# Optimization experiments

Hardware: AMD Instinct MI355X
Metric: run time of the kernel (lower is better)

## Reference

```python
import jax, jax.numpy as jnp
import numpy as np

HIDDEN = 1024
HEADS = 16
HEAD_DIM = HIDDEN // HEADS
ROPE_THETA = 10000.0
WINDOW = 128
NEG_INF = -1e9


def _rope_cos_sin(seq_len, head_dim, theta, dtype):
    # inv_freq: [dh/2]; emb = concat([freqs, freqs]) to match rotate-half convention
    inv_freq = 1.0 / (theta ** (jnp.arange(0, head_dim, 2, dtype=jnp.float32) / head_dim))
    pos = jnp.arange(seq_len, dtype=jnp.float32)
    freqs = jnp.einsum('s,d->sd', pos, inv_freq)          # [S, dh/2]
    emb = jnp.concatenate([freqs, freqs], axis=-1)        # [S, dh]
    return jnp.cos(emb).astype(dtype), jnp.sin(emb).astype(dtype)


def _apply_rope(x, cos, sin):
    # x: [B, S, H, dh]; cos/sin: [S, dh] broadcast over batch and heads
    x1, x2 = jnp.split(x, 2, axis=-1)
    half_rot = jnp.concatenate([-x2, x1], axis=-1)
    c = cos[None, :, None, :]
    s = sin[None, :, None, :]
    return x * c + half_rot * s


def setup_inputs() -> dict:
    key = jax.random.key(0)
    k1, k2, k3, k4, k5 = jax.random.split(key, 5)
    std = 0.02
    return {
        'hidden_states': jax.random.normal(k1, (2, 2048, HIDDEN), dtype=jnp.float32),
        'Wq': jax.random.normal(k2, (HIDDEN, HEADS, HEAD_DIM), dtype=jnp.float32) * std,
        'Wk': jax.random.normal(k3, (HIDDEN, HEADS, HEAD_DIM), dtype=jnp.float32) * std,
        'Wv': jax.random.normal(k4, (HIDDEN, HEADS, HEAD_DIM), dtype=jnp.float32) * std,
        'Wo': jax.random.normal(k5, (HEADS, HEAD_DIM, HIDDEN), dtype=jnp.float32) * std,
    }


def reference(hidden_states, Wq, Wk, Wv, Wo):
    B, S, D = hidden_states.shape
    x4 = hidden_states.reshape(B, S, HEADS, HEAD_DIM)
    cos, sin = _rope_cos_sin(S, HEAD_DIM, ROPE_THETA, hidden_states.dtype)
    # RoPE applied to raw hidden states (pre-projection), per original module
    q_in = _apply_rope(x4, cos, sin).reshape(B, S, D)
    k_in = q_in  # query and key get identical RoPE of the same tensor
    v_in = hidden_states

    q = jnp.einsum('bsd,dhk->bshk', q_in, Wq)  # [B,S,H,dh]
    k = jnp.einsum('bsd,dhk->bshk', k_in, Wk)
    v = jnp.einsum('bsd,dhk->bshk', v_in, Wv)

    scale = 1.0 / jnp.sqrt(jnp.asarray(HEAD_DIM, dtype=q.dtype))
    scores = jnp.einsum('bqhd,bkhd->bhqk', q, k) * scale  # [B,H,S,S]

    # sliding-window mask: |i - j| < WINDOW
    pos = jnp.arange(S)
    win = jnp.abs(pos[:, None] - pos[None, :]) < WINDOW   # [S,S] bool
    scores = jnp.where(win[None, None, :, :], scores, NEG_INF)

    probs = jax.nn.softmax(scores, axis=-1)
    out = jnp.einsum('bhqk,bkhd->bqhd', probs, v)          # [B,S,H,dh]
    return jnp.einsum('bqhd,hdo->bqo', out, Wo)            # [B,S,D]
```

## Files before the change

### kernel.cpp

```cpp
#include <hip/hip_runtime.h>
#include <hip/hip_bf16.h>
#include <cstdint>
#include <cmath>

typedef __bf16 bf16_t;
typedef __bf16 bf16x8 __attribute__((ext_vector_type(8)));
typedef __bf16 bf16x4 __attribute__((ext_vector_type(4)));
typedef float  f32x4  __attribute__((ext_vector_type(4)));

#define MFMA16(a, b, c) __builtin_amdgcn_mfma_f32_16x16x32_bf16(a, b, c, 0, 0, 0)

constexpr int   SS    = 2048;
constexpr int   DD    = 1024;
constexpr int   HH    = 16;
constexpr float SCALE = 0.125f;
constexpr float L2E   = 1.44269504088896f;

__device__ __forceinline__ bool detect_fp32(const uint16_t* w) {
    uint16_t v = w[threadIdx.x & 63];
    int e = (v >> 7) & 0xFF;
    unsigned long long m = __ballot(e >= 0x80);
    return __popcll(m) >= 4;
}

__device__ __forceinline__ float ldin(const void* p, size_t i, bool f32) {
    return f32 ? ((const float*)p)[i] : (float)((const bf16_t*)p)[i];
}

__device__ __forceinline__ void gload_lds16(const bf16_t* g, bf16_t* l) {
    __builtin_amdgcn_global_load_lds(
        (const __attribute__((address_space(1))) void*)(g),
        (__attribute__((address_space(3))) void*)(l), 16, 0, 0);
}

__global__ __launch_bounds__(256) void prep_kernel(
    const void* __restrict__ hidden, const void* __restrict__ Wq,
    const void* __restrict__ Wk, const void* __restrict__ Wv,
    const void* __restrict__ Wo,
    bf16_t* __restrict__ roped, bf16_t* __restrict__ hiddenb,
    bf16_t* __restrict__ WqT, bf16_t* __restrict__ WkT,
    bf16_t* __restrict__ WvT, bf16_t* __restrict__ WoT) {
    const bool f32 = detect_fp32((const uint16_t*)Wq);
    __shared__ bf16_t tile[32][33];
    if (blockIdx.x < 1024) {
        int gid = blockIdx.x * 256 + threadIdx.x;
        int ic = (gid & 3) * 8;
        int h  = (gid >> 2) & 15;
        int s  = (gid >> 6) & 2047;
        int b  = gid >> 17;
        size_t base = ((size_t)(b * SS + s)) * DD + h * 64 + ic;
        float x[8], y[8];
        if (f32) {
            const float* hp = (const float*)hidden;
            f32x4 x0 = *(const f32x4*)(hp + base);
            f32x4 x1 = *(const f32x4*)(hp + base + 4);
            f32x4 y0 = *(const f32x4*)(hp + base + 32);
            f32x4 y1 = *(const f32x4*)(hp + base + 36);
#pragma unroll
            for (int j = 0; j < 4; ++j) {
                x[j] = x0[j]; x[4 + j] = x1[j];
                y[j] = y0[j]; y[4 + j] = y1[j];
            }
        } else {
            const bf16_t* hp = (const bf16_t*)hidden;
            bf16x8 xv = *(const bf16x8*)(hp + base);
            bf16x8 yv = *(const bf16x8*)(hp + base + 32);
#pragma unroll
            for (int j = 0; j < 8; ++j) { x[j] = (float)xv[j]; y[j] = (float)yv[j]; }
        }
        bf16x8 ro, rh, hb0, hb1;
#pragma unroll
        for (int j = 0; j < 8; ++j) {
            int i = ic + j;
            float invf = exp2f(-(float)i * (13.287712379549449f / 32.0f));
            float sn, cs;
            __sincosf((float)s * invf, &sn, &cs);
            ro[j]  = (bf16_t)(x[j] * cs - y[j] * sn);
            rh[j]  = (bf16_t)(y[j] * cs + x[j] * sn);
            hb0[j] = (bf16_t)x[j];
            hb1[j] = (bf16_t)y[j];
        }
        *(bf16x8*)(roped + base)        = ro;
        *(bf16x8*)(roped + base + 32)   = rh;
        *(bf16x8*)(hiddenb + base)      = hb0;
        *(bf16x8*)(hiddenb + base + 32) = hb1;
    } else {
        int w = blockIdx.x - 1024;
        int z = w >> 10;
        int yy = (w >> 5) & 31, xx = w & 31;
        const void* src = (z == 0) ? Wq : (z == 1) ? Wk : (z == 2) ? Wv : Wo;
        bf16_t*     dst = (z == 0) ? WqT : (z == 1) ? WkT : (z == 2) ? WvT : WoT;
        int tx = threadIdx.x & 31, ty = threadIdx.x >> 5;
        int x0 = xx * 32, y0 = yy * 32;
#pragma unroll
        for (int j = 0; j < 4; ++j)
            tile[ty + j * 8][tx] =
                (bf16_t)ldin(src, (size_t)(y0 + ty + j * 8) * DD + x0 + tx, f32);
        __syncthreads();
#pragma unroll
        for (int j = 0; j < 4; ++j)
            dst[(size_t)(x0 + ty + j * 8) * DD + y0 + tx] = tile[tx][ty + j * 8];
    }
}

__device__ __forceinline__ void stage_a128(const bf16_t* A, int m0, int k0,
                                           bf16_t* As, int tid) {
#pragma unroll
    for (int i = 0; i < 4; ++i) {
        int c = tid + i * 256;
        gload_lds16(A + (size_t)(m0 + (c >> 3)) * DD + k0 + (c & 7) * 8, As + c * 8);
    }
}
__device__ __forceinline__ void stage_b64(const bf16_t* Bt, int n0, int k0,
                                          bf16_t* Bs, int tid) {
#pragma unroll
    for (int i = 0; i < 2; ++i) {
        int c = tid + i * 256;
        gload_lds16(Bt + (size_t)(n0 + (c >> 3)) * DD + k0 + (c & 7) * 8, Bs + c * 8);
    }
}

__global__ __launch_bounds__(256, 4) void gemm_qkv_fused(
    const bf16_t* __restrict__ roped, const bf16_t* __restrict__ hiddenb,
    const bf16_t* __restrict__ WqT, const bf16_t* __restrict__ WkT,
    const bf16_t* __restrict__ WvT,
    bf16_t* __restrict__ Qo, bf16_t* __restrict__ Ko, bf16_t* __restrict__ Vt) {
    __shared__ __align__(16) bf16_t As[128 * 64];
    __shared__ __align__(16) bf16_t B1[64 * 64];
    __shared__ __align__(16) bf16_t B2[64 * 64];
    const int tid = threadIdx.x, lane = tid & 63, quad = lane >> 4, l16 = lane & 15;
    const int wave = tid >> 6, wm = (wave >> 1) * 64, wn = (wave & 1) * 32;

    const int lin = blockIdx.x;
    const int xcd = lin & 7, s = lin >> 3;
    const int z = s >> 6, rem = s & 63;
    const int mb = (xcd >> 1) * 8 + (rem >> 3);
    const int nb = (xcd & 1) * 8 + (rem & 7);
    const int m0 = mb * 128, n0 = nb * 64;

    f32x4 acc1[4][2], acc2[4][2];
#pragma unroll
    for (int i = 0; i < 4; ++i)
#pragma unroll
        for (int j = 0; j < 2; ++j) { acc1[i][j] = (f32x4)0.0f; acc2[i][j] = (f32x4)0.0f; }

    if (z == 0) {
        for (int k0 = 0; k0 < DD; k0 += 64) {
            stage_a128(roped, m0, k0, As, tid);
            stage_b64(WqT, n0, k0, B1, tid);
            stage_b64(WkT, n0, k0, B2, tid);
            __syncthreads();
#pragma unroll
            for (int half = 0; half < 2; ++half) {
                bf16x8 af[4], b1f[2], b2f[2];
#pragma unroll
                for (int t = 0; t < 4; ++t)
                    af[t] = *(const bf16x8*)(As + (wm + t * 16 + l16) * 64 + half * 32 + quad * 8);
#pragma unroll
                for (int t = 0; t < 2; ++t) {
                    b1f[t] = *(const bf16x8*)(B1 + (wn + t * 16 + l16) * 64 + half * 32 + quad * 8);
                    b2f[t] = *(const bf16x8*)(B2 + (wn + t * 16 + l16) * 64 + half * 32 + quad * 8);
                }
#pragma unroll
                for (int i = 0; i < 4; ++i)
#pragma unroll
                    for (int j = 0; j < 2; ++j) {
                        acc1[i][j] = MFMA16(af[i], b1f[j], acc1[i][j]);
                        acc2[i][j] = MFMA16(af[i], b2f[j], acc2[i][j]);
                    }
            }
            __syncthreads();
        }
#pragma unroll
        for (int i = 0; i < 4; ++i) {
            int mbase = m0 + wm + i * 16 + quad * 4;
            int b = mbase >> 11, sl = mbase & 2047;
#pragma unroll
            for (int j = 0; j < 2; ++j) {
                int d = wn + j * 16 + l16;
                size_t base = (((size_t)b * HH + nb) * SS + sl) * 64 + d;
#pragma unroll
                for (int r = 0; r < 4; ++r) {
                    Qo[base + 64 * r] = (bf16_t)acc1[i][j][r];
                    Ko[base + 64 * r] = (bf16_t)acc2[i][j][r];
                }
            }
        }
    } else {
        for (int k0 = 0; k0 < DD; k0 += 64) {
            stage_a128(hiddenb, m0, k0, As, tid);
            stage_b64(WvT, n0, k0, B1, tid);
            __syncthreads();
#pragma unroll
            for (int half = 0; half < 2; ++half) {
                bf16x8 af[4], b1f[2];
#pragma unroll
                for (int t = 0; t < 4; ++t)
                    af[t] = *(const bf16x8*)(As + (wm + t * 16 + l16) * 64 + half * 32 + quad * 8);
#pragma unroll
                for (int t = 0; t < 2; ++t)
                    b1f[t] = *(const bf16x8*)(B1 + (wn + t * 16 + l16) * 64 + half * 32 + quad * 8);
#pragma unroll
                for (int i = 0; i < 4; ++i)
#pragma unroll
                    for (int j = 0; j < 2; ++j)
                        acc1[i][j] = MFMA16(af[i], b1f[j], acc1[i][j]);
            }
            __syncthreads();
        }
#pragma unroll
        for (int i = 0; i < 4; ++i) {
            int mbase = m0 + wm + i * 16 + quad * 4;
            int b = mbase >> 11, sl = mbase & 2047;
#pragma unroll
            for (int j = 0; j < 2; ++j) {
                int d = wn + j * 16 + l16;
                bf16x4 v;
                v[0] = (bf16_t)acc1[i][j][0]; v[1] = (bf16_t)acc1[i][j][1];
                v[2] = (bf16_t)acc1[i][j][2]; v[3] = (bf16_t)acc1[i][j][3];
                *(bf16x4*)(Vt + (((size_t)b * HH + nb) * 64 + d) * SS + sl) = v;
            }
        }
    }
}

__global__ __launch_bounds__(256) void attn_kernel(
    const bf16_t* __restrict__ Q, const bf16_t* __restrict__ Kk,
    const bf16_t* __restrict__ Vt, bf16_t* __restrict__ attn) {
    __shared__ __align__(16) bf16_t Ks[2][32 * 64];
    __shared__ __align__(16) bf16_t Vs[2][64 * 32];
    __shared__ __align__(16) bf16_t Pl[4][16 * 40];
    const int tid = threadIdx.x, wave = tid >> 6, lane = tid & 63;
    const int quad = lane >> 4, l16 = lane & 15;

    int lin = (blockIdx.x >> 3) + 128 * (blockIdx.x & 7);
    const int qb0 = (lin & 31) * 64;
    const int h   = (lin >> 5) & 15;
    const int b   = lin >> 9;
    const int qw  = qb0 + wave * 16;

    const size_t bh = (size_t)b * HH + h;
    const bf16_t* Qp = Q  + bh * SS * 64;
    const bf16_t* Kp = Kk + bh * SS * 64;
    const bf16_t* Vp = Vt + bh * 64 * SS;
    bf16_t* P = &Pl[wave][0];

    bf16x8 q0 = *(const bf16x8*)(Qp + (size_t)(qw + l16) * 64 + quad * 8);
    bf16x8 q1 = *(const bf16x8*)(Qp + (size_t)(qw + l16) * 64 + 32 + quad * 8);

    f32x4 Oacc[4];
#pragma unroll
    for (int t = 0; t < 4; ++t) Oacc[t] = (f32x4)0.0f;
    float lsum[4] = {0.f, 0.f, 0.f, 0.f};

    int lo = qb0 - 127; if (lo < 0) lo = 0; lo &= ~31;
    int hi = qb0 + 63 + 127; if (hi > SS - 1) hi = SS - 1;

    int parity = 0;
    for (int kt = lo; kt <= hi; kt += 32, parity ^= 1) {
        gload_lds16(Kp + (size_t)(kt + (tid >> 3)) * 64 + (tid & 7) * 8,
                    &Ks[parity][0] + tid * 8);
        gload_lds16(Vp + (size_t)(tid >> 2) * SS + kt + (tid & 3) * 8,
                    &Vs[parity][0] + tid * 8);
        __syncthreads();

        const bf16_t* Kl = &Ks[parity][0];
        const bf16_t* Vl = &Vs[parity][0];
        bf16x8 k00 = *(const bf16x8*)(Kl + l16 * 64 + quad * 8);
        bf16x8 k01 = *(const bf16x8*)(Kl + l16 * 64 + 32 + quad * 8);
        bf16x8 k10 = *(const bf16x8*)(Kl + (16 + l16) * 64 + quad * 8);
        bf16x8 k11 = *(const bf16x8*)(Kl + (16 + l16) * 64 + 32 + quad * 8);
        bf16x8 vf[4];
#pragma unroll
        for (int t = 0; t < 4; ++t)
            vf[t] = *(const bf16x8*)(Vl + (t * 16 + l16) * 32 + quad * 8);

        f32x4 s0 = MFMA16(q0, k00, (f32x4)0.0f);  s0 = MFMA16(q1, k01, s0);
        f32x4 s1 = MFMA16(q0, k10, (f32x4)0.0f);  s1 = MFMA16(q1, k11, s1);

        const int kr0 = kt + l16, kr1 = kt + 16 + l16;
#pragma unroll
        for (int r = 0; r < 4; ++r) {
            int qa = qw + quad * 4 + r;
            int d0 = qa - kr0; if (d0 < 0) d0 = -d0;
            int d1 = qa - kr1; if (d1 < 0) d1 = -d1;
            float p0 = (d0 < 128) ? exp2f(s0[r] * (SCALE * L2E)) : 0.0f;
            float p1 = (d1 < 128) ? exp2f(s1[r] * (SCALE * L2E)) : 0.0f;
            lsum[r] += p0 + p1;
            P[(quad * 4 + r) * 40 + l16]      = (bf16_t)p0;
            P[(quad * 4 + r) * 40 + 16 + l16] = (bf16_t)p1;
        }
        __asm__ volatile("s_waitcnt lgkmcnt(0)" ::: "memory");
        bf16x8 pf = *(const bf16x8*)(P + l16 * 40 + quad * 8);
#pragma unroll
        for (int t = 0; t < 4; ++t)
            Oacc[t] = MFMA16(pf, vf[t], Oacc[t]);
    }

#pragma unroll
    for (int r = 0; r < 4; ++r) {
        float l = lsum[r];
        l += __shfl_xor(l, 1, 64);
        l += __shfl_xor(l, 2, 64);
        l += __shfl_xor(l, 4, 64);
        l += __shfl_xor(l, 8, 64);
        float inv = 1.0f / l;
        int sa = qw + quad * 4 + r;
        size_t base = (((size_t)b * SS + sa) * HH + h) * 64 + l16;
        attn[base]      = (bf16_t)(Oacc[0][r] * inv);
        attn[base + 16] = (bf16_t)(Oacc[1][r] * inv);
        attn[base + 32] = (bf16_t)(Oacc[2][r] * inv);
        attn[base + 48] = (bf16_t)(Oacc[3][r] * inv);
    }
}

__global__ __launch_bounds__(256, 4) void gemm_out_kernel(
    const bf16_t* __restrict__ A, const bf16_t* __restrict__ WoT,
    const uint16_t* __restrict__ wdet, void* __restrict__ out) {
    __shared__ __align__(16) bf16_t As[128 * 64];
    __shared__ __align__(16) bf16_t B1[64 * 64];
    const int tid = threadIdx.x, lane = tid & 63, quad = lane >> 4, l16 = lane & 15;
    const int wave = tid >> 6, wm = (wave >> 1) * 64, wn = (wave & 1) * 32;

    const int lin = blockIdx.x;
    const int xcd = lin & 7, s = lin >> 3;
    const int mb = (xcd >> 1) * 8 + (s >> 3);
    const int nb = (xcd & 1) * 8 + (s & 7);
    const int m0 = mb * 128, n0 = nb * 64;

    f32x4 acc[4][2];
#pragma unroll
    for (int i = 0; i < 4; ++i)
#pragma unroll
        for (int j = 0; j < 2; ++j) acc[i][j] = (f32x4)0.0f;

    for (int k0 = 0; k0 < DD; k0 += 64) {
        stage_a128(A, m0, k0, As, tid);
        stage_b64(WoT, n0, k0, B1, tid);
        __syncthreads();
#pragma unroll
        for (int half = 0; half < 2; ++half) {
            bf16x8 af[4], b1f[2];
#pragma unroll
            for (int t = 0; t < 4; ++t)
                af[t] = *(const bf16x8*)(As + (wm + t * 16 + l16) * 64 + half * 32 + quad * 8);
#pragma unroll
            for (int t = 0; t < 2; ++t)
                b1f[t] = *(const bf16x8*)(B1 + (wn + t * 16 + l16) * 64 + half * 32 + quad * 8);
#pragma unroll
            for (int i = 0; i < 4; ++i)
#pragma unroll
                for (int j = 0; j < 2; ++j)
                    acc[i][j] = MFMA16(af[i], b1f[j], acc[i][j]);
        }
        __syncthreads();
    }

    const bool f32 = detect_fp32(wdet);
#pragma unroll
    for (int i = 0; i < 4; ++i) {
        int mbase = m0 + wm + i * 16 + quad * 4;
#pragma unroll
        for (int j = 0; j < 2; ++j) {
            int n = n0 + wn + j * 16 + l16;
#pragma unroll
            for (int r = 0; r < 4; ++r) {
                size_t idx = (size_t)(mbase + r) * DD + n;
                if (f32) ((float*)out)[idx] = acc[i][j][r];
                else     ((bf16_t*)out)[idx] = (bf16_t)acc[i][j][r];
            }
        }
    }
}

extern "C" void kernel_launch(void* const* d_in, const int* in_sizes, int n_in,
                              void* d_out, int out_size, void* d_ws, size_t ws_size,
                              hipStream_t stream) {
    const void* hidden = d_in[0];
    const void* Wq = d_in[1];
    const void* Wk = d_in[2];
    const void* Wv = d_in[3];
    const void* Wo = d_in[4];
    const uint16_t* wdet = (const uint16_t*)d_in[1];
    char* ws = (char*)d_ws;

    bf16_t* roped   = (bf16_t*)(ws);
    bf16_t* hiddenb = (bf16_t*)(ws + ( 8u << 20));
    bf16_t* WqT     = (bf16_t*)(ws + (16u << 20));
    bf16_t* WkT     = (bf16_t*)(ws + (18u << 20));
    bf16_t* WvT     = (bf16_t*)(ws + (20u << 20));
    bf16_t* WoT     = (bf16_t*)(ws + (22u << 20));
    bf16_t* Qb      = (bf16_t*)(ws + (24u << 20));
    bf16_t* Kb      = (bf16_t*)(ws + (32u << 20));
    bf16_t* Vt      = (bf16_t*)(ws + (40u << 20));
    bf16_t* attn    = roped;

    hipLaunchKernelGGL(prep_kernel, dim3(5120), dim3(256), 0, stream,
                       hidden, Wq, Wk, Wv, Wo, roped, hiddenb,
                       WqT, WkT, WvT, WoT);
    hipLaunchKernelGGL(gemm_qkv_fused, dim3(1024), dim3(256), 0, stream,
                       roped, hiddenb, WqT, WkT, WvT, Qb, Kb, Vt);
    hipLaunchKernelGGL(attn_kernel, dim3(1024), dim3(256), 0, stream,
                       Qb, Kb, Vt, attn);
    hipLaunchKernelGGL(gemm_out_kernel, dim3(512), dim3(256), 0, stream,
                       attn, WoT, wdet, d_out);
}
```

Baseline: 160.4 us.

## Widen attention key tiles to 64 with XOR-swizzled LDS and skip redundant bf16 copy

The attention kernel now processes 64 keys per iteration instead of 32, which halves the number of loop trips and barriers. K and V tiles are stored in LDS with an XOR swizzle to avoid bank conflicts, and the P buffer is widened to match. Separately, the prep kernel only writes the bf16 copy of the hidden states when the input is fp32, and the V GEMM otherwise reads the raw bf16 input directly. The trade-offs are more LDS per block, possibly lower occupancy, and more masked work at the window edges because of the coarser 64-key alignment.

```diff
diff --git a/kernel.cpp b/kernel.cpp
--- a/kernel.cpp
+++ b/kernel.cpp
@@ -68,7 +68,7 @@
 #pragma unroll
             for (int j = 0; j < 8; ++j) { x[j] = (float)xv[j]; y[j] = (float)yv[j]; }
         }
-        bf16x8 ro, rh, hb0, hb1;
+        bf16x8 ro, rh;
 #pragma unroll
         for (int j = 0; j < 8; ++j) {
             int i = ic + j;
@@ -77,13 +77,16 @@
             __sincosf((float)s * invf, &sn, &cs);
             ro[j]  = (bf16_t)(x[j] * cs - y[j] * sn);
             rh[j]  = (bf16_t)(y[j] * cs + x[j] * sn);
-            hb0[j] = (bf16_t)x[j];
-            hb1[j] = (bf16_t)y[j];
-        }
-        *(bf16x8*)(roped + base)        = ro;
-        *(bf16x8*)(roped + base + 32)   = rh;
-        *(bf16x8*)(hiddenb + base)      = hb0;
-        *(bf16x8*)(hiddenb + base + 32) = hb1;
+        }
+        *(bf16x8*)(roped + base)      = ro;
+        *(bf16x8*)(roped + base + 32) = rh;
+        if (f32) {
+            bf16x8 hb0, hb1;
+#pragma unroll
+            for (int j = 0; j < 8; ++j) { hb0[j] = (bf16_t)x[j]; hb1[j] = (bf16_t)y[j]; }
+            *(bf16x8*)(hiddenb + base)      = hb0;
+            *(bf16x8*)(hiddenb + base + 32) = hb1;
+        }
     } else {
         int w = blockIdx.x - 1024;
         int z = w >> 10;
@@ -121,7 +124,8 @@
 }
 
 __global__ __launch_bounds__(256, 4) void gemm_qkv_fused(
-    const bf16_t* __restrict__ roped, const bf16_t* __restrict__ hiddenb,
+    const bf16_t* __restrict__ roped, const void* __restrict__ hidden_raw,
+    const bf16_t* __restrict__ hiddenb, const uint16_t* __restrict__ wdet,
     const bf16_t* __restrict__ WqT, const bf16_t* __restrict__ WkT,
     const bf16_t* __restrict__ WvT,
     bf16_t* __restrict__ Qo, bf16_t* __restrict__ Ko, bf16_t* __restrict__ Vt) {
@@ -187,8 +191,10 @@
             }
         }
     } else {
+        const bool f32 = detect_fp32(wdet);
+        const bf16_t* A = f32 ? hiddenb : (const bf16_t*)hidden_raw;
         for (int k0 = 0; k0 < DD; k0 += 64) {
-            stage_a128(hiddenb, m0, k0, As, tid);
+            stage_a128(A, m0, k0, As, tid);
             stage_b64(WvT, n0, k0, B1, tid);
             __syncthreads();
 #pragma unroll
@@ -227,9 +233,9 @@
 __global__ __launch_bounds__(256) void attn_kernel(
     const bf16_t* __restrict__ Q, const bf16_t* __restrict__ Kk,
     const bf16_t* __restrict__ Vt, bf16_t* __restrict__ attn) {
-    __shared__ __align__(16) bf16_t Ks[2][32 * 64];
-    __shared__ __align__(16) bf16_t Vs[2][64 * 32];
-    __shared__ __align__(16) bf16_t Pl[4][16 * 40];
+    __shared__ __align__(16) bf16_t Ks[2][64 * 64];
+    __shared__ __align__(16) bf16_t Vs[2][64 * 64];
+    __shared__ __align__(16) bf16_t Pl[4][16 * 72];
     const int tid = threadIdx.x, wave = tid >> 6, lane = tid & 63;
     const int quad = lane >> 4, l16 = lane & 15;
 
@@ -253,48 +259,51 @@
     for (int t = 0; t < 4; ++t) Oacc[t] = (f32x4)0.0f;
     float lsum[4] = {0.f, 0.f, 0.f, 0.f};
 
-    int lo = qb0 - 127; if (lo < 0) lo = 0; lo &= ~31;
+    int lo = qb0 - 127; if (lo < 0) lo = 0; lo &= ~63;
     int hi = qb0 + 63 + 127; if (hi > SS - 1) hi = SS - 1;
 
+    const int c0 = tid, c1 = tid + 256;
+    const int r0 = c0 >> 3, g0 = (c0 & 7) ^ (r0 & 7);
+    const int r1 = c1 >> 3, g1 = (c1 & 7) ^ (r1 & 7);
+    const int sw = (l16 & 7);
+
     int parity = 0;
-    for (int kt = lo; kt <= hi; kt += 32, parity ^= 1) {
-        gload_lds16(Kp + (size_t)(kt + (tid >> 3)) * 64 + (tid & 7) * 8,
-                    &Ks[parity][0] + tid * 8);
-        gload_lds16(Vp + (size_t)(tid >> 2) * SS + kt + (tid & 3) * 8,
-                    &Vs[parity][0] + tid * 8);
+    for (int kt = lo; kt <= hi; kt += 64, parity ^= 1) {
+        gload_lds16(Kp + (size_t)(kt + r0) * 64 + g0 * 8, &Ks[parity][0] + c0 * 8);
+        gload_lds16(Kp + (size_t)(kt + r1) * 64 + g1 * 8, &Ks[parity][0] + c1 * 8);
+        gload_lds16(Vp + (size_t)r0 * SS + kt + g0 * 8, &Vs[parity][0] + c0 * 8);
+        gload_lds16(Vp + (size_t)r1 * SS + kt + g1 * 8, &Vs[parity][0] + c1 * 8);
         __syncthreads();
 
         const bf16_t* Kl = &Ks[parity][0];
         const bf16_t* Vl = &Vs[parity][0];
-        bf16x8 k00 = *(const bf16x8*)(Kl + l16 * 64 + quad * 8);
-        bf16x8 k01 = *(const bf16x8*)(Kl + l16 * 64 + 32 + quad * 8);
-        bf16x8 k10 = *(const bf16x8*)(Kl + (16 + l16) * 64 + quad * 8);
-        bf16x8 k11 = *(const bf16x8*)(Kl + (16 + l16) * 64 + 32 + quad * 8);
-        bf16x8 vf[4];
-#pragma unroll
-        for (int t = 0; t < 4; ++t)
-            vf[t] = *(const bf16x8*)(Vl + (t * 16 + l16) * 32 + quad * 8);
-
-        f32x4 s0 = MFMA16(q0, k00, (f32x4)0.0f);  s0 = MFMA16(q1, k01, s0);
-        f32x4 s1 = MFMA16(q0, k10, (f32x4)0.0f);  s1 = MFMA16(q1, k11, s1);
-
-        const int kr0 = kt + l16, kr1 = kt + 16 + l16;
-#pragma unroll
-        for (int r = 0; r < 4; ++r) {
-            int qa = qw + quad * 4 + r;
-            int d0 = qa - kr0; if (d0 < 0) d0 = -d0;
-            int d1 = qa - kr1; if (d1 < 0) d1 = -d1;
-            float p0 = (d0 < 128) ? exp2f(s0[r] * (SCALE * L2E)) : 0.0f;
-            float p1 = (d1 < 128) ? exp2f(s1[r] * (SCALE * L2E)) : 0.0f;
-            lsum[r] += p0 + p1;
-            P[(quad * 4 + r) * 40 + l16]      = (bf16_t)p0;
-            P[(quad * 4 + r) * 40 + 16 + l16] = (bf16_t)p1;
+
+#pragma unroll
+        for (int t = 0; t < 4; ++t) {
+            bf16x8 ka = *(const bf16x8*)(Kl + (t * 16 + l16) * 64 + (quad ^ sw) * 8);
+            bf16x8 kb = *(const bf16x8*)(Kl + (t * 16 + l16) * 64 + ((quad + 4) ^ sw) * 8);
+            f32x4 sc = MFMA16(q0, ka, (f32x4)0.0f);
+            sc = MFMA16(q1, kb, sc);
+            const int kr = kt + t * 16 + l16;
+#pragma unroll
+            for (int r = 0; r < 4; ++r) {
+                int qa = qw + quad * 4 + r;
+                int dd = qa - kr; if (dd < 0) dd = -dd;
+                float pv = (dd < 128) ? exp2f(sc[r] * (SCALE * L2E)) : 0.0f;
+                lsum[r] += pv;
+                P[(quad * 4 + r) * 72 + t * 16 + l16] = (bf16_t)pv;
+            }
         }
         __asm__ volatile("s_waitcnt lgkmcnt(0)" ::: "memory");
-        bf16x8 pf = *(const bf16x8*)(P + l16 * 40 + quad * 8);
-#pragma unroll
-        for (int t = 0; t < 4; ++t)
-            Oacc[t] = MFMA16(pf, vf[t], Oacc[t]);
+        bf16x8 pf0 = *(const bf16x8*)(P + l16 * 72 + quad * 8);
+        bf16x8 pf1 = *(const bf16x8*)(P + l16 * 72 + 32 + quad * 8);
+#pragma unroll
+        for (int t = 0; t < 4; ++t) {
+            bf16x8 va = *(const bf16x8*)(Vl + (t * 16 + l16) * 64 + (quad ^ sw) * 8);
+            bf16x8 vb = *(const bf16x8*)(Vl + (t * 16 + l16) * 64 + ((quad + 4) ^ sw) * 8);
+            Oacc[t] = MFMA16(pf0, va, Oacc[t]);
+            Oacc[t] = MFMA16(pf1, vb, Oacc[t]);
+        }
     }
 
 #pragma unroll
@@ -399,7 +408,7 @@
                        hidden, Wq, Wk, Wv, Wo, roped, hiddenb,
                        WqT, WkT, WvT, WoT);
     hipLaunchKernelGGL(gemm_qkv_fused, dim3(1024), dim3(256), 0, stream,
-                       roped, hiddenb, WqT, WkT, WvT, Qb, Kb, Vt);
+                       roped, hidden, hiddenb, wdet, WqT, WkT, WvT, Qb, Kb, Vt);
     hipLaunchKernelGGL(attn_kernel, dim3(1024), dim3(256), 0, stream,
                        Qb, Kb, Vt, attn);
     hipLaunchKernelGGL(gemm_out_kernel, dim3(512), dim3(256), 0, stream,
```

Result: slower. 165.0 us (+2.9%).
